# Optimization experiments

Measured on AMD Instinct MI355X. Metric: run time of the kernel, lower is better.

## Reference

```python
import jax, jax.numpy as jnp
import numpy as np

N_NODES = 100000
N_RADIAL = 16  # columns 0..15
N_CONICAL = 16  # columns 16..31


def setup_inputs() -> dict:
    key = jax.random.key(0)
    k1, k2, k3, k4 = jax.random.split(key, 4)
    x = jax.random.normal(k1, (N_NODES, 32), dtype=jnp.float32)
    edge_index = jax.random.randint(k2, (2, 1600000), 0, N_NODES, dtype=jnp.int32)
    W1 = jax.random.normal(k3, (32, 128), dtype=jnp.float32) * 0.1
    b1 = jnp.zeros((128,), dtype=jnp.float32)
    W2 = jax.random.normal(k4, (128, 32), dtype=jnp.float32) * 0.1
    b2 = jnp.zeros((32,), dtype=jnp.float32)
    return {"x": x, "edge_index": edge_index, "W1": W1, "b1": b1, "W2": W2, "b2": b2}


def reference(x, edge_index, W1, b1, W2, b2):
    # slice radial / conical feature channels
    radial = x[:, :N_RADIAL]            # [N, 16]
    conical = x[:, N_RADIAL:N_RADIAL + N_CONICAL]  # [N, 16]

    i, j = edge_index[0], edge_index[1]
    rows = jnp.concatenate([i, j])      # symmetrized COO rows [2E]
    cols = jnp.concatenate([j, i])      # symmetrized COO cols [2E]

    # coalesce()+sparse.mm == segment-sum over all (duplicated) entries
    neighbor_sum = jax.ops.segment_sum(conical[cols], rows, num_segments=N_NODES)  # [N, 16]
    deg = jax.ops.segment_sum(jnp.ones_like(rows, dtype=x.dtype), rows, num_segments=N_NODES)
    deg = jnp.clip(deg, 1.0)[:, None]   # bincount(...).clamp(min=1)
    agg = neighbor_sum / deg            # mean aggregation

    combined = jnp.concatenate([radial, agg], axis=1)  # [N, 32]
    h = jax.nn.relu(combined @ W1 + b1)
    out = h @ W2 + b2                   # [N, 32]
    return out
```

## Files before the change

### kernel.cpp

```cpp
#include <hip/hip_runtime.h>
#include <hip/hip_bf16.h>
#include <hip/hip_fp16.h>

#define N_NODES  100000
#define N_RADIAL 16
#define N_CONICAL 16

#define NPB    256
#define NBKT   ((N_NODES + NPB - 1) / NPB)
#define NBLK_A 256
#define BTHR   512
#define SUBCAP 96
#define BKTSTRIDE (NBLK_A * SUBCAP)
#define CAP    10240

__global__ __launch_bounds__(BTHR) void binfuse_kernel(
    const int* __restrict__ idx, const float* __restrict__ x,
    __half2* __restrict__ xcon2,
    const float* __restrict__ W1, const float* __restrict__ W2,
    float* __restrict__ W1t, float* __restrict__ W2t,
    unsigned int* __restrict__ binned, int* __restrict__ cnts,
    int chunk, int total, int E) {
    int b = blockIdx.x, tid = threadIdx.x;
    if (b >= NBLK_A) {
        int pb = b - NBLK_A;
        if (pb == 0) {
            for (int i = tid; i < 4096; i += BTHR) {
                int c = i >> 7, k = i & 127;
                W1t[k * 32 + c] = W1[i];
                int kk = i >> 5, o = i & 31;
                W2t[o * 128 + kk] = W2[i];
            }
        } else {
            int t = (pb - 1) * BTHR + tid;
            if (t < N_NODES * 8) {
                int n = t >> 3, p = t & 7;
                const float2* xp = (const float2*)x;
                float2 v = xp[n * 16 + 8 + p];
                xcon2[t] = __floats2half2_rn(v.x, v.y);
            }
        }
        return;
    }

    __shared__ int cur[NBKT];
    for (int i = tid; i < NBKT; i += BTHR)
        cur[i] = i * BKTSTRIDE + b * SUBCAP;
    __syncthreads();

    int lo = b * chunk;
    int hi = min(lo + chunk, total);
    for (int d = lo + tid; d < hi; d += BTHR) {
        int row = idx[d];
        int col = (d < E) ? idx[d + E] : idx[d - E];
        int bkt = row >> 8;
        int p = atomicAdd(&cur[bkt], 1);
        binned[p] = ((unsigned int)(row & 255) << 17) | (unsigned int)col;
    }
    __syncthreads();

    for (int i = tid; i < NBKT; i += BTHR)
        cnts[i * NBLK_A + b] = cur[i] - (i * BKTSTRIDE + b * SUBCAP);
}

__global__ __launch_bounds__(1024, 2) void agg_kernel(
    const __half* __restrict__ xcon, const int* __restrict__ cnts,
    const unsigned int* __restrict__ binned, __half* __restrict__ agg) {
    __shared__ unsigned int sedge[CAP];
    __shared__ int scnt[NPB];
    __shared__ int soff[NPB];
    int b = blockIdx.x, tid = threadIdx.x;
    if (tid < NPB) scnt[tid] = 0;
    __syncthreads();

    int sub = tid >> 2, l = tid & 2 * 2 - 1;
    int sc  = cnts[b * NBLK_A + sub];
    unsigned int base = (unsigned int)b * BKTSTRIDE + (unsigned int)sub * SUBCAP;

    for (int j = l; j < sc; j += 4)
        atomicAdd(&scnt[binned[base + j] >> 17], 1);
    __syncthreads();

    if (tid < NPB) soff[tid] = scnt[tid];
    __syncthreads();
    for (int off = 1; off < NPB; off <<= 1) {
        int y = 0;
        if (tid < NPB && tid >= off) y = soff[tid - off];
        __syncthreads();
        if (tid < NPB) soff[tid] += y;
        __syncthreads();
    }
    if (tid < NPB) soff[tid] -= scnt[tid];
    __syncthreads();

    for (int j = l; j < sc; j += 4) {
        unsigned int p = binned[base + j];
        int pos = atomicAdd(&soff[p >> 17], 1);
        sedge[pos] = p & 0x1FFFFu;
    }
    __syncthreads();

    if (tid < 2 * NPB) {
        int nl = tid >> 1, q = tid & 1;
        int c  = scnt[nl];
        int s0 = soff[nl] - c;
        float a0 = 0.f, a1 = 0.f, a2 = 0.f, a3 = 0.f;
        float a4 = 0.f, a5 = 0.f, a6 = 0.f, a7 = 0.f;
        #pragma unroll 2
        for (int k = 0; k < c; k++) {
            int col = (int)sedge[s0 + k];
            uint4 raw = ((const uint4*)(xcon + (size_t)col * 16))[q];
            float2 f0 = __half22float2(*(const __half2*)&raw.x);
            float2 f1 = __half22float2(*(const __half2*)&raw.y);
            float2 f2 = __half22float2(*(const __half2*)&raw.z);
            float2 f3 = __half22float2(*(const __half2*)&raw.w);
            a0 += f0.x; a1 += f0.y; a2 += f1.x; a3 += f1.y;
            a4 += f2.x; a5 += f2.y; a6 += f3.x; a7 += f3.y;
        }
        int n = b * NPB + nl;
        if (n < N_NODES) {
            float inv = 1.0f / (float)max(c, 1);
            __half2 h0 = __floats2half2_rn(a0 * inv, a1 * inv);
            __half2 h1 = __floats2half2_rn(a2 * inv, a3 * inv);
            __half2 h2 = __floats2half2_rn(a4 * inv, a5 * inv);
            __half2 h3 = __floats2half2_rn(a6 * inv, a7 * inv);
            uint4 st;
            st.x = *(unsigned int*)&h0; st.y = *(unsigned int*)&h1;
            st.z = *(unsigned int*)&h2; st.w = *(unsigned int*)&h3;
            *(uint4*)(agg + (size_t)n * 16 + q * 8) = st;
        }
    }
}

__global__ __launch_bounds__(512, 4) void mlp_kernel(
    const float* __restrict__ x, const __half* __restrict__ agg,
    const float* __restrict__ W1t, const float* __restrict__ b1,
    const float* __restrict__ W2t, const float* __restrict__ b2,
    float* __restrict__ out, int N) {
    __shared__ __half2 H2[64 * 64];
    int tid  = threadIdx.x;
    int lane = tid & 63;
    int ws   = __builtin_amdgcn_readfirstlane(tid >> 6);
    int n    = blockIdx.x * 64 + lane;
    int nc   = min(n, N - 1);

    float comb[32];
    const float4* xr = (const float4*)(x + (size_t)nc * 32);
    #pragma unroll
    for (int c = 0; c < 4; c++) {
        float4 v = xr[c];
        comb[c*4+0] = v.x; comb[c*4+1] = v.y;
        comb[c*4+2] = v.z; comb[c*4+3] = v.w;
    }
    const __half2* ar = (const __half2*)(agg + (size_t)nc * 16);
    #pragma unroll
    for (int c = 0; c < 8; c++) {
        float2 f = __half22float2(ar[c]);
        comb[16 + 2*c]     = f.x;
        comb[16 + 2*c + 1] = f.y;
    }

    #pragma unroll
    for (int i = 0; i < 16; i += 2) {
        int k0 = ws * 16 + i;
        const float* w1a = W1t + k0 * 32;
        const float* w1b = w1a + 32;
        float ha = b1[k0], hb = b1[k0 + 1];
        #pragma unroll
        for (int c = 0; c < 32; c++) {
            ha = fmaf(comb[c], w1a[c], ha);
            hb = fmaf(comb[c], w1b[c], hb);
        }
        ha = fmaxf(ha, 0.f); hb = fmaxf(hb, 0.f);
        H2[(k0 >> 1) * 64 + lane] = __floats2half2_rn(ha, hb);
    }
    __syncthreads();

    int o0 = ws * 4;
    const float* w20 = W2t + (o0 + 0) * 128;
    const float* w21 = W2t + (o0 + 1) * 128;
    const float* w22 = W2t + (o0 + 2) * 128;
    const float* w23 = W2t + (o0 + 3) * 128;
    float acc0 = b2[o0+0], acc1 = b2[o0+1], acc2 = b2[o0+2], acc3 = b2[o0+3];
    #pragma unroll 8
    for (int kp = 0; kp < 64; kp++) {
        float2 h = __half22float2(H2[kp * 64 + lane]);
        int k0 = 2 * kp;
        acc0 = fmaf(h.x, w20[k0], acc0); acc0 = fmaf(h.y, w20[k0+1], acc0);
        acc1 = fmaf(h.x, w21[k0], acc1); acc1 = fmaf(h.y, w21[k0+1], acc1);
        acc2 = fmaf(h.x, w22[k0], acc2); acc2 = fmaf(h.y, w22[k0+1], acc2);
        acc3 = fmaf(h.x, w23[k0], acc3); acc3 = fmaf(h.y, w23[k0+1], acc3);
    }
    if (n < N) {
        float* op = out + (size_t)n * 32 + o0;
        op[0] = acc0; op[1] = acc1; op[2] = acc2; op[3] = acc3;
    }
}

extern "C" void kernel_launch(void* const* d_in, const int* in_sizes, int n_in,
                              void* d_out, int out_size, void* d_ws, size_t ws_size,
                              hipStream_t stream) {
    const float* x   = (const float*)d_in[0];
    const int*   idx = (const int*)d_in[1];
    const float* W1  = (const float*)d_in[2];
    const float* b1  = (const float*)d_in[3];
    const float* W2  = (const float*)d_in[4];
    const float* b2  = (const float*)d_in[5];
    float* out = (float*)d_out;

    const int E = in_sizes[1] / 2;
    const int total = 2 * E;
    const int chunk = (total + NBLK_A - 1) / NBLK_A;

    char* base = (char*)d_ws;
    __half*       agg    = (__half*)base;
    __half*       xcon   = (__half*)(base + 3203072);
    float*        W1t    = (float*)(base + 6406144);
    float*        W2t    = (float*)(base + 6422528);
    int*          cnts   = (int*)(base + 6438912);
    unsigned int* binned = (unsigned int*)(base + 6839296);

    int pack_blocks = (N_NODES * 8 + BTHR - 1) / BTHR;
    binfuse_kernel<<<NBLK_A + 1 + pack_blocks, BTHR, 0, stream>>>(
        idx, x, (__half2*)xcon, W1, W2, W1t, W2t,
        binned, cnts, chunk, total, E);
    agg_kernel<<<NBKT, 1024, 0, stream>>>(xcon, cnts, binned, agg);
    mlp_kernel<<<(N_NODES + 63) / 64, 512, 0, stream>>>(
        x, agg, W1t, b1, W2t, b2, out, N_NODES);
}
```

Measured before the change: 160.0 us.

## Fuse aggregation and MLP into one kernel with smaller node buckets

Merges the aggregation and MLP kernels so each block gathers neighbor means for 128 nodes into shared memory and then runs the two-layer MLP on them directly. The fp16 agg round trip through global memory and one kernel launch go away. Bucket size, sub-bin capacity and binning block size are retuned to fit. The smaller SUBCAP of 64 per block per bucket raises the risk of overflowing binned slots, and the MLP now runs at the aggregation grid's occupancy.

```diff
diff --git a/kernel.cpp b/kernel.cpp
--- a/kernel.cpp
+++ b/kernel.cpp
@@ -6,15 +6,21 @@
 #define N_RADIAL 16
 #define N_CONICAL 16
 
-#define NPB    256
+#define NPB    128
 #define NBKT   ((N_NODES + NPB - 1) / NPB)
 #define NBLK_A 256
-#define BTHR   512
-#define SUBCAP 96
+#define BTHR   1024
+#define SUBCAP 64
 #define BKTSTRIDE (NBLK_A * SUBCAP)
-#define CAP    10240
-
-__global__ __launch_bounds__(BTHR) void binfuse_kernel(
+#define CAP    5120
+
+#define XCON_OFF   0u
+#define W1T_OFF    3200000u
+#define W2T_OFF    3216384u
+#define CNTS_OFF   3232768u
+#define BINNED_OFF 4033536u
+
+__global__ __launch_bounds__(BTHR, 2) void binfuse_kernel(
     const int* __restrict__ idx, const float* __restrict__ x,
     __half2* __restrict__ xcon2,
     const float* __restrict__ W1, const float* __restrict__ W2,
@@ -53,9 +59,9 @@
     for (int d = lo + tid; d < hi; d += BTHR) {
         int row = idx[d];
         int col = (d < E) ? idx[d + E] : idx[d - E];
-        int bkt = row >> 8;
+        int bkt = row >> 7;
         int p = atomicAdd(&cur[bkt], 1);
-        binned[p] = ((unsigned int)(row & 255) << 17) | (unsigned int)col;
+        binned[p] = ((unsigned int)(row & 127) << 17) | (unsigned int)col;
     }
     __syncthreads();
 
@@ -63,21 +69,28 @@
         cnts[i * NBLK_A + b] = cur[i] - (i * BKTSTRIDE + b * SUBCAP);
 }
 
-__global__ __launch_bounds__(1024, 2) void agg_kernel(
+__global__ __launch_bounds__(512, 4) void aggmlp_kernel(
     const __half* __restrict__ xcon, const int* __restrict__ cnts,
-    const unsigned int* __restrict__ binned, __half* __restrict__ agg) {
+    const unsigned int* __restrict__ binned,
+    const float* __restrict__ x,
+    const float* __restrict__ W1t, const float* __restrict__ b1,
+    const float* __restrict__ W2t, const float* __restrict__ b2,
+    float* __restrict__ out, int N) {
     __shared__ unsigned int sedge[CAP];
     __shared__ int scnt[NPB];
     __shared__ int soff[NPB];
+    __shared__ __half2 aggL[NPB * 8];
+    __half2* H2 = (__half2*)sedge;
+
     int b = blockIdx.x, tid = threadIdx.x;
     if (tid < NPB) scnt[tid] = 0;
     __syncthreads();
 
-    int sub = tid >> 2, l = tid & 2 * 2 - 1;
+    int sub = tid >> 1, l = tid & 1;
     int sc  = cnts[b * NBLK_A + sub];
     unsigned int base = (unsigned int)b * BKTSTRIDE + (unsigned int)sub * SUBCAP;
 
-    for (int j = l; j < sc; j += 4)
+    for (int j = l; j < sc; j += 2)
         atomicAdd(&scnt[binned[base + j] >> 17], 1);
     __syncthreads();
 
@@ -93,107 +106,91 @@
     if (tid < NPB) soff[tid] -= scnt[tid];
     __syncthreads();
 
-    for (int j = l; j < sc; j += 4) {
+    for (int j = l; j < sc; j += 2) {
         unsigned int p = binned[base + j];
         int pos = atomicAdd(&soff[p >> 17], 1);
         sedge[pos] = p & 0x1FFFFu;
     }
     __syncthreads();
 
-    if (tid < 2 * NPB) {
-        int nl = tid >> 1, q = tid & 1;
+    {
+        int nl = tid >> 2, q = tid & 3;
         int c  = scnt[nl];
         int s0 = soff[nl] - c;
         float a0 = 0.f, a1 = 0.f, a2 = 0.f, a3 = 0.f;
-        float a4 = 0.f, a5 = 0.f, a6 = 0.f, a7 = 0.f;
-        #pragma unroll 2
+        #pragma unroll 4
         for (int k = 0; k < c; k++) {
             int col = (int)sedge[s0 + k];
-            uint4 raw = ((const uint4*)(xcon + (size_t)col * 16))[q];
+            uint2 raw = ((const uint2*)(xcon + (size_t)col * 16))[q];
             float2 f0 = __half22float2(*(const __half2*)&raw.x);
             float2 f1 = __half22float2(*(const __half2*)&raw.y);
-            float2 f2 = __half22float2(*(const __half2*)&raw.z);
-            float2 f3 = __half22float2(*(const __half2*)&raw.w);
             a0 += f0.x; a1 += f0.y; a2 += f1.x; a3 += f1.y;
-            a4 += f2.x; a5 += f2.y; a6 += f3.x; a7 += f3.y;
-        }
-        int n = b * NPB + nl;
-        if (n < N_NODES) {
-            float inv = 1.0f / (float)max(c, 1);
-            __half2 h0 = __floats2half2_rn(a0 * inv, a1 * inv);
-            __half2 h1 = __floats2half2_rn(a2 * inv, a3 * inv);
-            __half2 h2 = __floats2half2_rn(a4 * inv, a5 * inv);
-            __half2 h3 = __floats2half2_rn(a6 * inv, a7 * inv);
-            uint4 st;
-            st.x = *(unsigned int*)&h0; st.y = *(unsigned int*)&h1;
-            st.z = *(unsigned int*)&h2; st.w = *(unsigned int*)&h3;
-            *(uint4*)(agg + (size_t)n * 16 + q * 8) = st;
-        }
-    }
-}
-
-__global__ __launch_bounds__(512, 4) void mlp_kernel(
-    const float* __restrict__ x, const __half* __restrict__ agg,
-    const float* __restrict__ W1t, const float* __restrict__ b1,
-    const float* __restrict__ W2t, const float* __restrict__ b2,
-    float* __restrict__ out, int N) {
-    __shared__ __half2 H2[64 * 64];
-    int tid  = threadIdx.x;
+        }
+        float inv = 1.0f / (float)max(c, 1);
+        aggL[nl * 8 + q * 2]     = __floats2half2_rn(a0 * inv, a1 * inv);
+        aggL[nl * 8 + q * 2 + 1] = __floats2half2_rn(a2 * inv, a3 * inv);
+    }
+    __syncthreads();
+
     int lane = tid & 63;
     int ws   = __builtin_amdgcn_readfirstlane(tid >> 6);
-    int n    = blockIdx.x * 64 + lane;
-    int nc   = min(n, N - 1);
-
-    float comb[32];
-    const float4* xr = (const float4*)(x + (size_t)nc * 32);
     #pragma unroll
-    for (int c = 0; c < 4; c++) {
-        float4 v = xr[c];
-        comb[c*4+0] = v.x; comb[c*4+1] = v.y;
-        comb[c*4+2] = v.z; comb[c*4+3] = v.w;
-    }
-    const __half2* ar = (const __half2*)(agg + (size_t)nc * 16);
-    #pragma unroll
-    for (int c = 0; c < 8; c++) {
-        float2 f = __half22float2(ar[c]);
-        comb[16 + 2*c]     = f.x;
-        comb[16 + 2*c + 1] = f.y;
-    }
-
-    #pragma unroll
-    for (int i = 0; i < 16; i += 2) {
-        int k0 = ws * 16 + i;
-        const float* w1a = W1t + k0 * 32;
-        const float* w1b = w1a + 32;
-        float ha = b1[k0], hb = b1[k0 + 1];
+    for (int t = 0; t < 2; t++) {
+        int nlocal = t * 64 + lane;
+        int n  = b * NPB + nlocal;
+        int nc = min(n, N - 1);
+
+        float comb[32];
+        const float4* xr = (const float4*)(x + (size_t)nc * 32);
         #pragma unroll
-        for (int c = 0; c < 32; c++) {
-            ha = fmaf(comb[c], w1a[c], ha);
-            hb = fmaf(comb[c], w1b[c], hb);
-        }
-        ha = fmaxf(ha, 0.f); hb = fmaxf(hb, 0.f);
-        H2[(k0 >> 1) * 64 + lane] = __floats2half2_rn(ha, hb);
-    }
-    __syncthreads();
-
-    int o0 = ws * 4;
-    const float* w20 = W2t + (o0 + 0) * 128;
-    const float* w21 = W2t + (o0 + 1) * 128;
-    const float* w22 = W2t + (o0 + 2) * 128;
-    const float* w23 = W2t + (o0 + 3) * 128;
-    float acc0 = b2[o0+0], acc1 = b2[o0+1], acc2 = b2[o0+2], acc3 = b2[o0+3];
-    #pragma unroll 8
-    for (int kp = 0; kp < 64; kp++) {
-        float2 h = __half22float2(H2[kp * 64 + lane]);
-        int k0 = 2 * kp;
-        acc0 = fmaf(h.x, w20[k0], acc0); acc0 = fmaf(h.y, w20[k0+1], acc0);
-        acc1 = fmaf(h.x, w21[k0], acc1); acc1 = fmaf(h.y, w21[k0+1], acc1);
-        acc2 = fmaf(h.x, w22[k0], acc2); acc2 = fmaf(h.y, w22[k0+1], acc2);
-        acc3 = fmaf(h.x, w23[k0], acc3); acc3 = fmaf(h.y, w23[k0+1], acc3);
-    }
-    if (n < N) {
-        float* op = out + (size_t)n * 32 + o0;
-        op[0] = acc0; op[1] = acc1; op[2] = acc2; op[3] = acc3;
+        for (int c = 0; c < 4; c++) {
+            float4 v = xr[c];
+            comb[c*4+0] = v.x; comb[c*4+1] = v.y;
+            comb[c*4+2] = v.z; comb[c*4+3] = v.w;
+        }
+        #pragma unroll
+        for (int c = 0; c < 8; c++) {
+            float2 f = __half22float2(aggL[nlocal * 8 + c]);
+            comb[16 + 2*c]     = f.x;
+            comb[16 + 2*c + 1] = f.y;
+        }
+
+        #pragma unroll
+        for (int i = 0; i < 16; i += 2) {
+            int k0 = ws * 16 + i;
+            const float* w1a = W1t + k0 * 32;
+            const float* w1b = w1a + 32;
+            float ha = b1[k0], hb = b1[k0 + 1];
+            #pragma unroll
+            for (int c = 0; c < 32; c++) {
+                ha = fmaf(comb[c], w1a[c], ha);
+                hb = fmaf(comb[c], w1b[c], hb);
+            }
+            ha = fmaxf(ha, 0.f); hb = fmaxf(hb, 0.f);
+            H2[(k0 >> 1) * 64 + lane] = __floats2half2_rn(ha, hb);
+        }
+        __syncthreads();
+
+        int o0 = ws * 4;
+        const float* w20 = W2t + (o0 + 0) * 128;
+        const float* w21 = W2t + (o0 + 1) * 128;
+        const float* w22 = W2t + (o0 + 2) * 128;
+        const float* w23 = W2t + (o0 + 3) * 128;
+        float acc0 = b2[o0+0], acc1 = b2[o0+1], acc2 = b2[o0+2], acc3 = b2[o0+3];
+        #pragma unroll 8
+        for (int kp = 0; kp < 64; kp++) {
+            float2 h = __half22float2(H2[kp * 64 + lane]);
+            int k0 = 2 * kp;
+            acc0 = fmaf(h.x, w20[k0], acc0); acc0 = fmaf(h.y, w20[k0+1], acc0);
+            acc1 = fmaf(h.x, w21[k0], acc1); acc1 = fmaf(h.y, w21[k0+1], acc1);
+            acc2 = fmaf(h.x, w22[k0], acc2); acc2 = fmaf(h.y, w22[k0+1], acc2);
+            acc3 = fmaf(h.x, w23[k0], acc3); acc3 = fmaf(h.y, w23[k0+1], acc3);
+        }
+        if (n < N) {
+            float* op = out + (size_t)n * 32 + o0;
+            op[0] = acc0; op[1] = acc1; op[2] = acc2; op[3] = acc3;
+        }
+        __syncthreads();
     }
 }
 
@@ -213,18 +210,16 @@
     const int chunk = (total + NBLK_A - 1) / NBLK_A;
 
     char* base = (char*)d_ws;
-    __half*       agg    = (__half*)base;
-    __half*       xcon   = (__half*)(base + 3203072);
-    float*        W1t    = (float*)(base + 6406144);
-    float*        W2t    = (float*)(base + 6422528);
-    int*          cnts   = (int*)(base + 6438912);
-    unsigned int* binned = (unsigned int*)(base + 6839296);
+    __half*       xcon   = (__half*)(base + XCON_OFF);
+    float*        W1t    = (float*)(base + W1T_OFF);
+    float*        W2t    = (float*)(base + W2T_OFF);
+    int*          cnts   = (int*)(base + CNTS_OFF);
+    unsigned int* binned = (unsigned int*)(base + BINNED_OFF);
 
     int pack_blocks = (N_NODES * 8 + BTHR - 1) / BTHR;
     binfuse_kernel<<<NBLK_A + 1 + pack_blocks, BTHR, 0, stream>>>(
         idx, x, (__half2*)xcon, W1, W2, W1t, W2t,
         binned, cnts, chunk, total, E);
-    agg_kernel<<<NBKT, 1024, 0, stream>>>(xcon, cnts, binned, agg);
-    mlp_kernel<<<(N_NODES + 63) / 64, 512, 0, stream>>>(
-        x, agg, W1t, b1, W2t, b2, out, N_NODES);
+    aggmlp_kernel<<<NBKT, 512, 0, stream>>>(
+        xcon, cnts, binned, x, W1t, b1, W2t, b2, out, N_NODES);
 }
```

Result: slower. 183.5 us (+14.7%).

## Replace per-bucket count+scan with fixed-stride two-pass node slots in aggregation

Applied to the files above, without the earlier changes.

The aggregation kernel no longer counts edges per node and runs a shared-memory prefix scan. It processes each 256-node bucket in two halves of 128 nodes, scattering edges into fixed 97-entry slots per node with atomic cursors. The gather now uses 4 threads per node with 8-byte loads instead of 2 threads with 16-byte loads, which raises parallelism in the accumulation phase. Bounds clamps are added in binning and aggregation, so edges beyond the caps would be silently dropped, and each block now reads its binned edges twice.

```diff
diff --git a/kernel.cpp b/kernel.cpp
--- a/kernel.cpp
+++ b/kernel.cpp
@@ -12,7 +12,15 @@
 #define BTHR   512
 #define SUBCAP 96
 #define BKTSTRIDE (NBLK_A * SUBCAP)
-#define CAP    10240
+#define HNODES 128
+#define NSTRIDE 97
+
+#define AGG_OFF    0u
+#define XCON_OFF   3203072u
+#define W1T_OFF    6406144u
+#define W2T_OFF    6422528u
+#define CNTS_OFF   6438912u
+#define BINNED_OFF 6839296u
 
 __global__ __launch_bounds__(BTHR) void binfuse_kernel(
     const int* __restrict__ idx, const float* __restrict__ x,
@@ -55,80 +63,68 @@
         int col = (d < E) ? idx[d + E] : idx[d - E];
         int bkt = row >> 8;
         int p = atomicAdd(&cur[bkt], 1);
-        binned[p] = ((unsigned int)(row & 255) << 17) | (unsigned int)col;
+        if (p < bkt * BKTSTRIDE + b * SUBCAP + SUBCAP)
+            binned[p] = ((unsigned int)(row & 255) << 17) | (unsigned int)col;
     }
     __syncthreads();
 
     for (int i = tid; i < NBKT; i += BTHR)
-        cnts[i * NBLK_A + b] = cur[i] - (i * BKTSTRIDE + b * SUBCAP);
+        cnts[i * NBLK_A + b] =
+            min(cur[i] - (i * BKTSTRIDE + b * SUBCAP), SUBCAP);
 }
 
 __global__ __launch_bounds__(1024, 2) void agg_kernel(
     const __half* __restrict__ xcon, const int* __restrict__ cnts,
     const unsigned int* __restrict__ binned, __half* __restrict__ agg) {
-    __shared__ unsigned int sedge[CAP];
-    __shared__ int scnt[NPB];
-    __shared__ int soff[NPB];
+    __shared__ unsigned int sedge[HNODES * NSTRIDE];
+    __shared__ int cur[HNODES];
     int b = blockIdx.x, tid = threadIdx.x;
-    if (tid < NPB) scnt[tid] = 0;
-    __syncthreads();
-
-    int sub = tid >> 2, l = tid & 2 * 2 - 1;
-    int sc  = cnts[b * NBLK_A + sub];
+
+    int sub = tid >> 2, l = tid & 3;
+    int sc  = min(cnts[b * NBLK_A + sub], SUBCAP);
     unsigned int base = (unsigned int)b * BKTSTRIDE + (unsigned int)sub * SUBCAP;
 
-    for (int j = l; j < sc; j += 4)
-        atomicAdd(&scnt[binned[base + j] >> 17], 1);
-    __syncthreads();
-
-    if (tid < NPB) soff[tid] = scnt[tid];
-    __syncthreads();
-    for (int off = 1; off < NPB; off <<= 1) {
-        int y = 0;
-        if (tid < NPB && tid >= off) y = soff[tid - off];
+    for (int h = 0; h < 2; h++) {
+        if (tid < HNODES) cur[tid] = tid * NSTRIDE;
         __syncthreads();
-        if (tid < NPB) soff[tid] += y;
+
+        for (int j = l; j < sc; j += 4) {
+            unsigned int p = binned[base + j];
+            int rl = (int)(p >> 17);
+            if ((rl >> 7) == h) {
+                int nl = rl & 127;
+                int pos = atomicAdd(&cur[nl], 1);
+                if (pos < nl * NSTRIDE + NSTRIDE)
+                    sedge[pos] = p & 0x1FFFFu;
+            }
+        }
         __syncthreads();
-    }
-    if (tid < NPB) soff[tid] -= scnt[tid];
-    __syncthreads();
-
-    for (int j = l; j < sc; j += 4) {
-        unsigned int p = binned[base + j];
-        int pos = atomicAdd(&soff[p >> 17], 1);
-        sedge[pos] = p & 0x1FFFFu;
-    }
-    __syncthreads();
-
-    if (tid < 2 * NPB) {
-        int nl = tid >> 1, q = tid & 1;
-        int c  = scnt[nl];
-        int s0 = soff[nl] - c;
-        float a0 = 0.f, a1 = 0.f, a2 = 0.f, a3 = 0.f;
-        float a4 = 0.f, a5 = 0.f, a6 = 0.f, a7 = 0.f;
-        #pragma unroll 2
-        for (int k = 0; k < c; k++) {
-            int col = (int)sedge[s0 + k];
-            uint4 raw = ((const uint4*)(xcon + (size_t)col * 16))[q];
-            float2 f0 = __half22float2(*(const __half2*)&raw.x);
-            float2 f1 = __half22float2(*(const __half2*)&raw.y);
-            float2 f2 = __half22float2(*(const __half2*)&raw.z);
-            float2 f3 = __half22float2(*(const __half2*)&raw.w);
-            a0 += f0.x; a1 += f0.y; a2 += f1.x; a3 += f1.y;
-            a4 += f2.x; a5 += f2.y; a6 += f3.x; a7 += f3.y;
-        }
-        int n = b * NPB + nl;
-        if (n < N_NODES) {
-            float inv = 1.0f / (float)max(c, 1);
-            __half2 h0 = __floats2half2_rn(a0 * inv, a1 * inv);
-            __half2 h1 = __floats2half2_rn(a2 * inv, a3 * inv);
-            __half2 h2 = __floats2half2_rn(a4 * inv, a5 * inv);
-            __half2 h3 = __floats2half2_rn(a6 * inv, a7 * inv);
-            uint4 st;
-            st.x = *(unsigned int*)&h0; st.y = *(unsigned int*)&h1;
-            st.z = *(unsigned int*)&h2; st.w = *(unsigned int*)&h3;
-            *(uint4*)(agg + (size_t)n * 16 + q * 8) = st;
-        }
+
+        if (tid < 4 * HNODES) {
+            int nl = tid >> 2, q = tid & 3;
+            int c  = min(cur[nl] - nl * NSTRIDE, NSTRIDE);
+            int s0 = nl * NSTRIDE;
+            float a0 = 0.f, a1 = 0.f, a2 = 0.f, a3 = 0.f;
+            #pragma unroll 4
+            for (int k = 0; k < c; k++) {
+                int col = (int)sedge[s0 + k];
+                uint2 raw = ((const uint2*)(xcon + (size_t)col * 16))[q];
+                float2 f0 = __half22float2(*(const __half2*)&raw.x);
+                float2 f1 = __half22float2(*(const __half2*)&raw.y);
+                a0 += f0.x; a1 += f0.y; a2 += f1.x; a3 += f1.y;
+            }
+            int n = b * NPB + h * HNODES + nl;
+            if (n < N_NODES) {
+                float inv = 1.0f / (float)max(c, 1);
+                __half2 h0 = __floats2half2_rn(a0 * inv, a1 * inv);
+                __half2 h1 = __floats2half2_rn(a2 * inv, a3 * inv);
+                uint2 st;
+                st.x = *(unsigned int*)&h0;
+                st.y = *(unsigned int*)&h1;
+                *(uint2*)(agg + (size_t)n * 16 + q * 4) = st;
+            }
+        }
+        __syncthreads();
     }
 }
 
@@ -213,12 +209,12 @@
     const int chunk = (total + NBLK_A - 1) / NBLK_A;
 
     char* base = (char*)d_ws;
-    __half*       agg    = (__half*)base;
-    __half*       xcon   = (__half*)(base + 3203072);
-    float*        W1t    = (float*)(base + 6406144);
-    float*        W2t    = (float*)(base + 6422528);
-    int*          cnts   = (int*)(base + 6438912);
-    unsigned int* binned = (unsigned int*)(base + 6839296);
+    __half*       agg    = (__half*)(base + AGG_OFF);
+    __half*       xcon   = (__half*)(base + XCON_OFF);
+    float*        W1t    = (float*)(base + W1T_OFF);
+    float*        W2t    = (float*)(base + W2T_OFF);
+    int*          cnts   = (int*)(base + CNTS_OFF);
+    unsigned int* binned = (unsigned int*)(base + BINNED_OFF);
 
     int pack_blocks = (N_NODES * 8 + BTHR - 1) / BTHR;
     binfuse_kernel<<<NBLK_A + 1 + pack_blocks, BTHR, 0, stream>>>(
```

Measured after the change: 166.7 us. 4.2% more time.
